# Kernel optimization log

Measured on AMD Instinct MI355X. Metric: run time of the kernel, lower is better.

Reference implementation:

```python
import jax, jax.numpy as jnp
import numpy as np

B, NQ, N, D_IN, D_KEY, D_MODEL = 8, 2048, 2048, 512, 512, 512


def setup_inputs() -> dict:
    key = jax.random.key(0)
    k1, k2, k3, k4, k5, k6 = jax.random.split(key, 6)
    lim_k = np.sqrt(6.0 / (D_IN + D_KEY))
    lim_v = np.sqrt(6.0 / (D_IN + D_MODEL))
    return {
        "node_features": jax.random.normal(k1, (B, N, D_IN), dtype=jnp.float32),
        "query": jax.random.normal(k2, (B, NQ, D_IN), dtype=jnp.float32),
        "mask": jax.random.bernoulli(k3, 0.3, (NQ, B, N)),  # True = masked out
        "wq": jax.random.uniform(k4, (D_IN, D_KEY), jnp.float32, -lim_k, lim_k),
        "wk": jax.random.uniform(k5, (D_IN, D_KEY), jnp.float32, -lim_k, lim_k),
        "wv": jax.random.uniform(k6, (D_IN, D_MODEL), jnp.float32, -lim_v, lim_v),
    }


def reference(node_features, query, mask, wq, wk, wv):
    # Projections
    Q = query @ wq              # [B, NQ, d_key]
    K = node_features @ wk      # [B, N, d_key]
    V = node_features @ wv      # [B, N, d_model]
    # Raw scores [B, NQ, N]
    scores = jnp.einsum("bqd,bnd->bqn", Q, K)
    b, nq, n = scores.shape
    # Faithful to tf: reshape to (NQ, B, N), mask with float32.min, reshape back
    s = scores.reshape(nq, b, n)
    masked = jnp.where(mask, jnp.finfo(jnp.float32).min, s).reshape(b, nq, n)
    # Scale AFTER masking (as in the original), then softmax over keys
    attn = jax.nn.softmax(masked / jnp.sqrt(jnp.float32(K.shape[-1])), axis=-1)
    return attn @ V             # [B, NQ, d_model]
```

## Files before the change

### kernel.cpp

```cpp
#include <hip/hip_runtime.h>

#define BATCH 8
#define NQ    2048
#define NKV   2048
#define DIN   512
#define DKEY  512
#define DMOD  512

typedef __attribute__((ext_vector_type(8))) short bf16x8;
typedef __attribute__((ext_vector_type(4))) float f32x4;

__device__ __forceinline__ unsigned short f2bf(float f) {
  unsigned int u = __builtin_bit_cast(unsigned int, f);
  u += 0x7fffu + ((u >> 16) & 1u);
  return (unsigned short)(u >> 16);
}
__device__ __forceinline__ float bf2f(unsigned short h) {
  unsigned int u = ((unsigned int)h) << 16;
  return __builtin_bit_cast(float, u);
}

#define GLD16(gp, lp) __builtin_amdgcn_global_load_lds( \
    (const __attribute__((address_space(1))) unsigned int*)(gp), \
    (__attribute__((address_space(3))) unsigned int*)(lp), 16, 0, 0)

__global__ void detect_mode(const unsigned int* __restrict__ mask, int* __restrict__ flag) {
  __shared__ int c1s;
  if (threadIdx.x == 0) c1s = 0;
  __syncthreads();
  int c1 = 0;
  for (int i = threadIdx.x; i < 16384; i += 256) {
    unsigned int u = mask[i];
    if (u & 0x0000ff00u) c1++;
  }
  atomicAdd(&c1s, c1);
  __syncthreads();
  if (threadIdx.x == 0) *flag = (c1s > 0) ? 1 : 4;
}

__global__ void cvt_two(const float* __restrict__ a, const float* __restrict__ b,
                        unsigned short* __restrict__ oa, unsigned short* __restrict__ ob) {
  int i = blockIdx.x * 256 + threadIdx.x;
  const float* src;
  unsigned short* dst;
  int j;
  if (i < 2097152) { src = a; dst = oa; j = i; }
  else             { src = b; dst = ob; j = i - 2097152; }
  float4 v = ((const float4*)src)[j];
  ushort4 o;
  o.x = f2bf(v.x); o.y = f2bf(v.y); o.z = f2bf(v.z); o.w = f2bf(v.w);
  ((ushort4*)dst)[j] = o;
}

__global__ void cvt_w3(const float* __restrict__ wq, const float* __restrict__ wk,
                       const float* __restrict__ wv,
                       unsigned short* __restrict__ oq, unsigned short* __restrict__ ok,
                       unsigned short* __restrict__ ov) {
  int idx = blockIdx.x * 256 + threadIdx.x;
  int w = idx >> 18;
  int rem = idx & 262143;
  int n = rem >> 9, k = rem & 511;
  const float* W = (w == 0) ? wq : (w == 1) ? wk : wv;
  unsigned short* O = (w == 0) ? oq : (w == 1) ? ok : ov;
  O[n * 512 + k] = f2bf(W[k * 512 + n]);
}

__device__ __forceinline__ void gemm256_core(
    const unsigned short* __restrict__ Ab,
    const unsigned short* __restrict__ Bb,
    unsigned short* __restrict__ C,
    long ldA, long ldB, long ldO, int nk, long bm, long bn, char* smem)
{
  const int tid = threadIdx.x;
  const int lane = tid & 63;
  const int wid = tid >> 6;
  const int wr = wid >> 1;
  const int wc = wid & 1;
  const int fr = lane & 15, fq = lane >> 4;

  const int srow = tid >> 3;
  const int clog = (tid & 7) ^ (srow & 7);

  char* buf0 = smem;
  char* buf1 = smem + 65536;

  f32x4 acc[4][8] = {};

  const int swz0 = ((fq)     ^ (fr & 7)) * 16;
  const int swz1 = ((4 + fq) ^ (fr & 7)) * 16;
  const int arow = (wr * 64 + fr) * 128;
  const int brow = (wc * 128 + fr) * 128;

  {
    const unsigned short* ga = Ab + (bm + srow) * ldA + clog * 8;
    const unsigned short* gb = Bb + (bn + srow) * ldB + clog * 8;
#pragma unroll
    for (int l = 0; l < 4; ++l) {
      GLD16(ga + (long)l * 64 * ldA, buf0 + l * 8192 + tid * 16);
      GLD16(gb + (long)l * 64 * ldB, buf0 + 32768 + l * 8192 + tid * 16);
    }
  }

  char* cur = buf0;
  char* nxt = buf1;
  for (int t = 0; t < nk; ++t) {
    __builtin_amdgcn_sched_barrier(0);
    __builtin_amdgcn_s_barrier();
    if (t + 1 < nk) {
      const long k0 = (long)(t + 1) * 64;
      const unsigned short* ga = Ab + (bm + srow) * ldA + k0 + clog * 8;
      const unsigned short* gb = Bb + (bn + srow) * ldB + k0 + clog * 8;
#pragma unroll
      for (int l = 0; l < 4; ++l) {
        GLD16(ga + (long)l * 64 * ldA, nxt + l * 8192 + tid * 16);
        GLD16(gb + (long)l * 64 * ldB, nxt + 32768 + l * 8192 + tid * 16);
      }
      asm volatile("s_waitcnt vmcnt(8)" ::: "memory");
    } else {
      asm volatile("s_waitcnt vmcnt(0)" ::: "memory");
    }
    __builtin_amdgcn_s_barrier();
    __builtin_amdgcn_sched_barrier(0);

    const char* bufA = cur;
    const char* bufB = cur + 32768;
#pragma unroll
    for (int kh = 0; kh < 2; ++kh) {
      const int swz = kh ? swz1 : swz0;
      bf16x8 a[4];
#pragma unroll
      for (int mi = 0; mi < 4; ++mi)
        a[mi] = *(const bf16x8*)(bufA + arow + mi * 2048 + swz);
#pragma unroll
      for (int nh = 0; nh < 2; ++nh) {
        bf16x8 b[4];
#pragma unroll
        for (int nj = 0; nj < 4; ++nj)
          b[nj] = *(const bf16x8*)(bufB + brow + (nh * 4 + nj) * 2048 + swz);
        __builtin_amdgcn_s_setprio(1);
#pragma unroll
        for (int mi = 0; mi < 4; ++mi)
#pragma unroll
          for (int nj = 0; nj < 4; ++nj)
            acc[mi][nh * 4 + nj] = __builtin_amdgcn_mfma_f32_16x16x32_bf16(
                a[mi], b[nj], acc[mi][nh * 4 + nj], 0, 0, 0);
        __builtin_amdgcn_s_setprio(0);
      }
    }
    char* tmp = cur; cur = nxt; nxt = tmp;
  }

#pragma unroll
  for (int mi = 0; mi < 4; ++mi)
#pragma unroll
    for (int ni = 0; ni < 8; ++ni) {
      const long row = bm + wr * 64 + mi * 16 + fq * 4;
      const long col = bn + wc * 128 + ni * 16 + fr;
#pragma unroll
      for (int r = 0; r < 4; ++r)
        C[(row + r) * ldO + col] = f2bf(acc[mi][ni][r]);
    }
}

__global__ __launch_bounds__(512, 2) void gemm256_scores(
    const unsigned short* __restrict__ Q, const unsigned short* __restrict__ Kb,
    unsigned short* __restrict__ S)
{
  extern __shared__ char smem[];
  const long z = blockIdx.z;
  gemm256_core(Q + z * 1048576, Kb + z * 1048576, S + z * 4194304,
               512, 512, 2048, 8, (long)blockIdx.x * 256, (long)blockIdx.y * 256, smem);
}

__global__ __launch_bounds__(512, 2) void gemm256_proj(
    const unsigned short* __restrict__ Xq, const unsigned short* __restrict__ Xn,
    const unsigned short* __restrict__ Wqt, const unsigned short* __restrict__ Wkt,
    const unsigned short* __restrict__ Wvt,
    unsigned short* __restrict__ Q, unsigned short* __restrict__ Kb,
    unsigned short* __restrict__ Vt)
{
  extern __shared__ char smem[];
  const int z = blockIdx.z;
  if (z == 0)
    gemm256_core(Xq, Wqt, Q, 512, 512, 512, 8,
                 (long)blockIdx.x * 256, (long)blockIdx.y * 256, smem);
  else if (z == 1)
    gemm256_core(Xn, Wkt, Kb, 512, 512, 512, 8,
                 (long)blockIdx.x * 256, (long)blockIdx.y * 256, smem);
  else
    gemm256_core(Wvt, Xn, Vt, 512, 512, 16384, 8,
                 (long)blockIdx.y * 256, (long)blockIdx.x * 256, smem);
}

__device__ __forceinline__ void gemm_core(
    const unsigned short* Ab, const unsigned short* Bb, void* Cb,
    int K, long ldB, int out_mode, long ldO, long bm, long bn,
    unsigned short (*Al)[32], unsigned short (*Bl)[32])
{
  const int t = threadIdx.x;
  const int lane = t & 63;
  const int w = t >> 6;
  const int wm = (w >> 1) * 64, wn = (w & 1) * 64;
  const int fr = lane & 15, fq = lane >> 4;

  f32x4 acc[4][4] = {};

  const int slot0 = t, slot1 = 256 + t;
  const int r0 = slot0 >> 2, s0 = slot0 & 3;
  const int r1 = slot1 >> 2, s1 = slot1 & 3;

  const int nk = K >> 5;
  for (int kt = 0; kt < nk; ++kt) {
    const long k0 = (long)kt << 5;
    GLD16(Ab + (bm + r0) * K + k0 + s0 * 8, &Al[0][0] + slot0 * 8);
    GLD16(Ab + (bm + r1) * K + k0 + s1 * 8, &Al[0][0] + slot1 * 8);
    GLD16(Bb + (bn + r0) * ldB + k0 + s0 * 8, &Bl[0][0] + slot0 * 8);
    GLD16(Bb + (bn + r1) * ldB + k0 + s1 * 8, &Bl[0][0] + slot1 * 8);
    __syncthreads();

    bf16x8 af[4], bfr[4];
#pragma unroll
    for (int mi = 0; mi < 4; ++mi)
      af[mi] = *(const bf16x8*)&Al[wm + mi * 16 + fr][fq * 8];
#pragma unroll
    for (int ni = 0; ni < 4; ++ni)
      bfr[ni] = *(const bf16x8*)&Bl[wn + ni * 16 + fr][fq * 8];
#pragma unroll
    for (int mi = 0; mi < 4; ++mi)
#pragma unroll
      for (int ni = 0; ni < 4; ++ni)
        acc[mi][ni] = __builtin_amdgcn_mfma_f32_16x16x32_bf16(af[mi], bfr[ni], acc[mi][ni], 0, 0, 0);
    __syncthreads();
  }

  if (out_mode == 2) {
    float* C = (float*)Cb;
#pragma unroll
    for (int mi = 0; mi < 4; ++mi)
#pragma unroll
      for (int ni = 0; ni < 4; ++ni) {
        const long row = bm + wm + mi * 16 + fq * 4;
        const long col = bn + wn + ni * 16 + fr;
#pragma unroll
        for (int r = 0; r < 4; ++r)
          C[(row + r) * ldO + col] = acc[mi][ni][r];
      }
  } else {
    unsigned short* C = (unsigned short*)Cb;
#pragma unroll
    for (int mi = 0; mi < 4; ++mi)
#pragma unroll
      for (int ni = 0; ni < 4; ++ni) {
        const long row = bm + wm + mi * 16 + fq * 4;
        const long col = bn + wn + ni * 16 + fr;
#pragma unroll
        for (int r = 0; r < 4; ++r)
          C[(row + r) * ldO + col] = f2bf(acc[mi][ni][r]);
      }
  }
}

__global__ __launch_bounds__(256) void gemm_bt(
    const unsigned short* __restrict__ A,
    const unsigned short* __restrict__ Bt,
    void* __restrict__ Cout,
    int K, long ldB,
    long batchA, long batchB, long batchC,
    int out_mode, long ldO, int out_f32)
{
  __shared__ unsigned short Al[128][32];
  __shared__ unsigned short Bl[128][32];
  const unsigned short* Ab = A + (size_t)blockIdx.z * batchA;
  const unsigned short* Bb = Bt + (size_t)blockIdx.z * batchB;
  char* Cb = (char*)Cout + (size_t)blockIdx.z * batchC * (out_f32 ? 4 : 2);
  gemm_core(Ab, Bb, Cb, K, ldB, out_mode, ldO,
            (long)blockIdx.x * 128, (long)blockIdx.y * 128, Al, Bl);
}

__global__ __launch_bounds__(256) void softmax_rows(
    unsigned short* __restrict__ S,
    const unsigned char* __restrict__ mask,
    const int* __restrict__ flag)
{
  const int t = threadIdx.x;
  const size_t base = (size_t)blockIdx.x * 2048 + (size_t)t * 8;
  uint4 sv = *(const uint4*)(S + base);

  float x[8];
  {
    unsigned int w0 = sv.x, w1 = sv.y, w2 = sv.z, w3 = sv.w;
    x[0] = bf2f((unsigned short)(w0 & 0xffff)); x[1] = bf2f((unsigned short)(w0 >> 16));
    x[2] = bf2f((unsigned short)(w1 & 0xffff)); x[3] = bf2f((unsigned short)(w1 >> 16));
    x[4] = bf2f((unsigned short)(w2 & 0xffff)); x[5] = bf2f((unsigned short)(w2 >> 16));
    x[6] = bf2f((unsigned short)(w3 & 0xffff)); x[7] = bf2f((unsigned short)(w3 >> 16));
  }

  const int esz = *flag;
  unsigned int mbits = 0;
  if (esz == 1) {
    unsigned long long mv = *(const unsigned long long*)(mask + base);
#pragma unroll
    for (int j = 0; j < 8; ++j)
      if ((mv >> (8 * j)) & 0xffULL) mbits |= 1u << j;
  } else {
    const uint4* mp = (const uint4*)(mask + base * 4);
    uint4 a = mp[0], b = mp[1];
    if (a.x) mbits |= 1u;   if (a.y) mbits |= 2u;
    if (a.z) mbits |= 4u;   if (a.w) mbits |= 8u;
    if (b.x) mbits |= 16u;  if (b.y) mbits |= 32u;
    if (b.z) mbits |= 64u;  if (b.w) mbits |= 128u;
  }

  const float SCALE = 0.04419417382415922f;
  float xs[8];
#pragma unroll
  for (int j = 0; j < 8; ++j) {
    float v = ((mbits >> j) & 1u) ? -3.4028234663852886e38f : x[j];
    xs[j] = v * SCALE;
  }

  float m = xs[0];
#pragma unroll
  for (int j = 1; j < 8; ++j) m = fmaxf(m, xs[j]);
#pragma unroll
  for (int off = 32; off > 0; off >>= 1) m = fmaxf(m, __shfl_xor(m, off));

  __shared__ float rm[4], rs[4];
  if ((t & 63) == 0) rm[t >> 6] = m;
  __syncthreads();
  m = fmaxf(fmaxf(rm[0], rm[1]), fmaxf(rm[2], rm[3]));

  float e[8], ssum = 0.f;
#pragma unroll
  for (int j = 0; j < 8; ++j) { e[j] = __expf(xs[j] - m); ssum += e[j]; }
#pragma unroll
  for (int off = 32; off > 0; off >>= 1) ssum += __shfl_xor(ssum, off);
  if ((t & 63) == 0) rs[t >> 6] = ssum;
  __syncthreads();
  ssum = rs[0] + rs[1] + rs[2] + rs[3];
  const float inv = 1.0f / ssum;

  unsigned int o0 = (unsigned int)f2bf(e[0] * inv) | ((unsigned int)f2bf(e[1] * inv) << 16);
  unsigned int o1 = (unsigned int)f2bf(e[2] * inv) | ((unsigned int)f2bf(e[3] * inv) << 16);
  unsigned int o2 = (unsigned int)f2bf(e[4] * inv) | ((unsigned int)f2bf(e[5] * inv) << 16);
  unsigned int o3 = (unsigned int)f2bf(e[6] * inv) | ((unsigned int)f2bf(e[7] * inv) << 16);
  uint4 ov; ov.x = o0; ov.y = o1; ov.z = o2; ov.w = o3;
  *(uint4*)(S + base) = ov;
}

extern "C" void kernel_launch(void* const* d_in, const int* in_sizes, int n_in,
                              void* d_out, int out_size, void* d_ws, size_t ws_size,
                              hipStream_t stream) {
  const float* node  = (const float*)d_in[0];
  const float* query = (const float*)d_in[1];
  const unsigned char* mask = (const unsigned char*)d_in[2];
  const float* wq = (const float*)d_in[3];
  const float* wk = (const float*)d_in[4];
  const float* wv = (const float*)d_in[5];
  float* out = (float*)d_out;

  char* ws = (char*)d_ws;
  unsigned short* Q   = (unsigned short*)(ws);
  unsigned short* Kb  = (unsigned short*)(ws + 16777216);
  unsigned short* Vt  = (unsigned short*)(ws + 33554432);
  unsigned short* S   = (unsigned short*)(ws + 50331648);
  unsigned short* Xq  = (unsigned short*)(ws + 50331648);
  unsigned short* Xn  = (unsigned short*)(ws + 50331648 + 16777216);
  unsigned short* Wqt = (unsigned short*)(ws + 50331648 + 33554432);
  unsigned short* Wkt = Wqt + 262144;
  unsigned short* Wvt = Wkt + 262144;
  int* flag = (int*)(ws + 117440512);

  detect_mode<<<1, 256, 0, stream>>>((const unsigned int*)mask, flag);

  cvt_two<<<16384, 256, 0, stream>>>(query, node, Xq, Xn);
  cvt_w3<<<3072, 256, 0, stream>>>(wq, wk, wv, Wqt, Wkt, Wvt);

  dim3 gp(64, 2, 3);
  gemm256_proj<<<gp, 512, 131072, stream>>>(Xq, Xn, Wqt, Wkt, Wvt, Q, Kb, Vt);

  dim3 gs(8, 8, 8);
  gemm256_scores<<<gs, 512, 131072, stream>>>(Q, Kb, S);

  softmax_rows<<<16384, 256, 0, stream>>>(S, mask, flag);

  dim3 gv(16, 4, 8);
  gemm_bt<<<gv, 256, 0, stream>>>(S, Vt, out, 2048, 16384,
                                  4194304L, 2048L, 1048576L, 2, 512, 1);
}
```

Measured before the change: 220.9 us.

## Fuse mask and exp into scores GEMM epilogue, defer normalization to PV GEMM

The scores GEMM epilogue now applies the mask and writes exp(score*scale) directly, skipping the max subtraction. A light rowsum kernel computes reciprocal row sums. A new double-buffered 256x128 PV GEMM applies those reciprocals in its epilogue, replacing the separate softmax pass and the older gemm_bt kernel. This removes a full read-modify-write pass over the score matrix. The cost is that exp without max subtraction can overflow for large scores, and a fully masked row would give NaN where the reference gives a uniform row.

```diff
diff --git a/kernel.cpp b/kernel.cpp
--- a/kernel.cpp
+++ b/kernel.cpp
@@ -14,10 +14,6 @@
   unsigned int u = __builtin_bit_cast(unsigned int, f);
   u += 0x7fffu + ((u >> 16) & 1u);
   return (unsigned short)(u >> 16);
-}
-__device__ __forceinline__ float bf2f(unsigned short h) {
-  unsigned int u = ((unsigned int)h) << 16;
-  return __builtin_bit_cast(float, u);
 }
 
 #define GLD16(gp, lp) __builtin_amdgcn_global_load_lds( \
@@ -69,7 +65,8 @@
     const unsigned short* __restrict__ Ab,
     const unsigned short* __restrict__ Bb,
     unsigned short* __restrict__ C,
-    long ldA, long ldB, long ldO, int nk, long bm, long bn, char* smem)
+    long ldA, long ldB, long ldO, int nk, long bm, long bn, char* smem,
+    const unsigned char* emask, int esz, long maskBase)
 {
   const int tid = threadIdx.x;
   const int lane = tid & 63;
@@ -150,26 +147,41 @@
     char* tmp = cur; cur = nxt; nxt = tmp;
   }
 
+  const float SCALE = 0.04419417382415922f;
 #pragma unroll
   for (int mi = 0; mi < 4; ++mi)
 #pragma unroll
     for (int ni = 0; ni < 8; ++ni) {
       const long row = bm + wr * 64 + mi * 16 + fq * 4;
       const long col = bn + wc * 128 + ni * 16 + fr;
-#pragma unroll
-      for (int r = 0; r < 4; ++r)
-        C[(row + r) * ldO + col] = f2bf(acc[mi][ni][r]);
+      if (emask == nullptr) {
+#pragma unroll
+        for (int r = 0; r < 4; ++r)
+          C[(row + r) * ldO + col] = f2bf(acc[mi][ni][r]);
+      } else {
+#pragma unroll
+        for (int r = 0; r < 4; ++r) {
+          const long f = maskBase + (row + r) * ldO + col;
+          bool msk;
+          if (esz == 1) msk = emask[f] != 0;
+          else          msk = ((const unsigned int*)emask)[f] != 0;
+          float e = msk ? 0.0f : __expf(acc[mi][ni][r] * SCALE);
+          C[(row + r) * ldO + col] = f2bf(e);
+        }
+      }
     }
 }
 
 __global__ __launch_bounds__(512, 2) void gemm256_scores(
     const unsigned short* __restrict__ Q, const unsigned short* __restrict__ Kb,
-    unsigned short* __restrict__ S)
+    unsigned short* __restrict__ S,
+    const unsigned char* __restrict__ mask, const int* __restrict__ flag)
 {
   extern __shared__ char smem[];
   const long z = blockIdx.z;
   gemm256_core(Q + z * 1048576, Kb + z * 1048576, S + z * 4194304,
-               512, 512, 2048, 8, (long)blockIdx.x * 256, (long)blockIdx.y * 256, smem);
+               512, 512, 2048, 8, (long)blockIdx.x * 256, (long)blockIdx.y * 256, smem,
+               mask, *flag, z * 4194304);
 }
 
 __global__ __launch_bounds__(512, 2) void gemm256_proj(
@@ -183,169 +195,137 @@
   const int z = blockIdx.z;
   if (z == 0)
     gemm256_core(Xq, Wqt, Q, 512, 512, 512, 8,
-                 (long)blockIdx.x * 256, (long)blockIdx.y * 256, smem);
+                 (long)blockIdx.x * 256, (long)blockIdx.y * 256, smem, nullptr, 0, 0);
   else if (z == 1)
     gemm256_core(Xn, Wkt, Kb, 512, 512, 512, 8,
-                 (long)blockIdx.x * 256, (long)blockIdx.y * 256, smem);
+                 (long)blockIdx.x * 256, (long)blockIdx.y * 256, smem, nullptr, 0, 0);
   else
     gemm256_core(Wvt, Xn, Vt, 512, 512, 16384, 8,
-                 (long)blockIdx.y * 256, (long)blockIdx.x * 256, smem);
-}
-
-__device__ __forceinline__ void gemm_core(
-    const unsigned short* Ab, const unsigned short* Bb, void* Cb,
-    int K, long ldB, int out_mode, long ldO, long bm, long bn,
-    unsigned short (*Al)[32], unsigned short (*Bl)[32])
-{
-  const int t = threadIdx.x;
-  const int lane = t & 63;
-  const int w = t >> 6;
-  const int wm = (w >> 1) * 64, wn = (w & 1) * 64;
+                 (long)blockIdx.y * 256, (long)blockIdx.x * 256, smem, nullptr, 0, 0);
+}
+
+__global__ __launch_bounds__(256) void rowsum_inv(
+    const unsigned short* __restrict__ E, float* __restrict__ inv)
+{
+  const int row = blockIdx.x * 4 + (threadIdx.x >> 6);
+  const int lane = threadIdx.x & 63;
+  const uint4* p = (const uint4*)(E + (size_t)row * 2048);
+  float s = 0.f;
+#pragma unroll
+  for (int j = 0; j < 4; ++j) {
+    uint4 v = p[lane + j * 64];
+    unsigned int w[4] = {v.x, v.y, v.z, v.w};
+#pragma unroll
+    for (int q = 0; q < 4; ++q) {
+      s += __builtin_bit_cast(float, (w[q] & 0xffffu) << 16);
+      s += __builtin_bit_cast(float, w[q] & 0xffff0000u);
+    }
+  }
+#pragma unroll
+  for (int off = 32; off > 0; off >>= 1) s += __shfl_xor(s, off);
+  if (lane == 0) inv[row] = 1.0f / s;
+}
+
+__global__ __launch_bounds__(512, 2) void gemm_pv(
+    const unsigned short* __restrict__ E, const unsigned short* __restrict__ Vt,
+    const float* __restrict__ inv, float* __restrict__ O)
+{
+  extern __shared__ char smem[];
+  const long z = blockIdx.z;
+  const unsigned short* Ab = E + z * 4194304;
+  const unsigned short* Bb = Vt + z * 2048;
+  const long bm = (long)blockIdx.x * 256;
+  const long bn = (long)blockIdx.y * 128;
+
+  const int tid = threadIdx.x;
+  const int lane = tid & 63;
+  const int wid = tid >> 6;
+  const int wr = wid >> 1;
+  const int wc = wid & 1;
   const int fr = lane & 15, fq = lane >> 4;
 
+  const int srow = tid >> 3;
+  const int clog = (tid & 7) ^ (srow & 7);
+
+  char* buf0 = smem;
+  char* buf1 = smem + 49152;
+
   f32x4 acc[4][4] = {};
 
-  const int slot0 = t, slot1 = 256 + t;
-  const int r0 = slot0 >> 2, s0 = slot0 & 3;
-  const int r1 = slot1 >> 2, s1 = slot1 & 3;
-
-  const int nk = K >> 5;
-  for (int kt = 0; kt < nk; ++kt) {
-    const long k0 = (long)kt << 5;
-    GLD16(Ab + (bm + r0) * K + k0 + s0 * 8, &Al[0][0] + slot0 * 8);
-    GLD16(Ab + (bm + r1) * K + k0 + s1 * 8, &Al[0][0] + slot1 * 8);
-    GLD16(Bb + (bn + r0) * ldB + k0 + s0 * 8, &Bl[0][0] + slot0 * 8);
-    GLD16(Bb + (bn + r1) * ldB + k0 + s1 * 8, &Bl[0][0] + slot1 * 8);
-    __syncthreads();
-
-    bf16x8 af[4], bfr[4];
-#pragma unroll
-    for (int mi = 0; mi < 4; ++mi)
-      af[mi] = *(const bf16x8*)&Al[wm + mi * 16 + fr][fq * 8];
-#pragma unroll
-    for (int ni = 0; ni < 4; ++ni)
-      bfr[ni] = *(const bf16x8*)&Bl[wn + ni * 16 + fr][fq * 8];
-#pragma unroll
-    for (int mi = 0; mi < 4; ++mi)
-#pragma unroll
-      for (int ni = 0; ni < 4; ++ni)
-        acc[mi][ni] = __builtin_amdgcn_mfma_f32_16x16x32_bf16(af[mi], bfr[ni], acc[mi][ni], 0, 0, 0);
-    __syncthreads();
-  }
-
-  if (out_mode == 2) {
-    float* C = (float*)Cb;
-#pragma unroll
-    for (int mi = 0; mi < 4; ++mi)
-#pragma unroll
-      for (int ni = 0; ni < 4; ++ni) {
-        const long row = bm + wm + mi * 16 + fq * 4;
-        const long col = bn + wn + ni * 16 + fr;
-#pragma unroll
-        for (int r = 0; r < 4; ++r)
-          C[(row + r) * ldO + col] = acc[mi][ni][r];
-      }
-  } else {
-    unsigned short* C = (unsigned short*)Cb;
-#pragma unroll
-    for (int mi = 0; mi < 4; ++mi)
-#pragma unroll
-      for (int ni = 0; ni < 4; ++ni) {
-        const long row = bm + wm + mi * 16 + fq * 4;
-        const long col = bn + wn + ni * 16 + fr;
-#pragma unroll
-        for (int r = 0; r < 4; ++r)
-          C[(row + r) * ldO + col] = f2bf(acc[mi][ni][r]);
-      }
-  }
-}
-
-__global__ __launch_bounds__(256) void gemm_bt(
-    const unsigned short* __restrict__ A,
-    const unsigned short* __restrict__ Bt,
-    void* __restrict__ Cout,
-    int K, long ldB,
-    long batchA, long batchB, long batchC,
-    int out_mode, long ldO, int out_f32)
-{
-  __shared__ unsigned short Al[128][32];
-  __shared__ unsigned short Bl[128][32];
-  const unsigned short* Ab = A + (size_t)blockIdx.z * batchA;
-  const unsigned short* Bb = Bt + (size_t)blockIdx.z * batchB;
-  char* Cb = (char*)Cout + (size_t)blockIdx.z * batchC * (out_f32 ? 4 : 2);
-  gemm_core(Ab, Bb, Cb, K, ldB, out_mode, ldO,
-            (long)blockIdx.x * 128, (long)blockIdx.y * 128, Al, Bl);
-}
-
-__global__ __launch_bounds__(256) void softmax_rows(
-    unsigned short* __restrict__ S,
-    const unsigned char* __restrict__ mask,
-    const int* __restrict__ flag)
-{
-  const int t = threadIdx.x;
-  const size_t base = (size_t)blockIdx.x * 2048 + (size_t)t * 8;
-  uint4 sv = *(const uint4*)(S + base);
-
-  float x[8];
+  const int swz0 = ((fq)     ^ (fr & 7)) * 16;
+  const int swz1 = ((4 + fq) ^ (fr & 7)) * 16;
+  const int arow = (wr * 64 + fr) * 128;
+  const int brow = (wc * 64 + fr) * 128;
+
   {
-    unsigned int w0 = sv.x, w1 = sv.y, w2 = sv.z, w3 = sv.w;
-    x[0] = bf2f((unsigned short)(w0 & 0xffff)); x[1] = bf2f((unsigned short)(w0 >> 16));
-    x[2] = bf2f((unsigned short)(w1 & 0xffff)); x[3] = bf2f((unsigned short)(w1 >> 16));
-    x[4] = bf2f((unsigned short)(w2 & 0xffff)); x[5] = bf2f((unsigned short)(w2 >> 16));
-    x[6] = bf2f((unsigned short)(w3 & 0xffff)); x[7] = bf2f((unsigned short)(w3 >> 16));
-  }
-
-  const int esz = *flag;
-  unsigned int mbits = 0;
-  if (esz == 1) {
-    unsigned long long mv = *(const unsigned long long*)(mask + base);
-#pragma unroll
-    for (int j = 0; j < 8; ++j)
-      if ((mv >> (8 * j)) & 0xffULL) mbits |= 1u << j;
-  } else {
-    const uint4* mp = (const uint4*)(mask + base * 4);
-    uint4 a = mp[0], b = mp[1];
-    if (a.x) mbits |= 1u;   if (a.y) mbits |= 2u;
-    if (a.z) mbits |= 4u;   if (a.w) mbits |= 8u;
-    if (b.x) mbits |= 16u;  if (b.y) mbits |= 32u;
-    if (b.z) mbits |= 64u;  if (b.w) mbits |= 128u;
-  }
-
-  const float SCALE = 0.04419417382415922f;
-  float xs[8];
-#pragma unroll
-  for (int j = 0; j < 8; ++j) {
-    float v = ((mbits >> j) & 1u) ? -3.4028234663852886e38f : x[j];
-    xs[j] = v * SCALE;
-  }
-
-  float m = xs[0];
-#pragma unroll
-  for (int j = 1; j < 8; ++j) m = fmaxf(m, xs[j]);
-#pragma unroll
-  for (int off = 32; off > 0; off >>= 1) m = fmaxf(m, __shfl_xor(m, off));
-
-  __shared__ float rm[4], rs[4];
-  if ((t & 63) == 0) rm[t >> 6] = m;
-  __syncthreads();
-  m = fmaxf(fmaxf(rm[0], rm[1]), fmaxf(rm[2], rm[3]));
-
-  float e[8], ssum = 0.f;
-#pragma unroll
-  for (int j = 0; j < 8; ++j) { e[j] = __expf(xs[j] - m); ssum += e[j]; }
-#pragma unroll
-  for (int off = 32; off > 0; off >>= 1) ssum += __shfl_xor(ssum, off);
-  if ((t & 63) == 0) rs[t >> 6] = ssum;
-  __syncthreads();
-  ssum = rs[0] + rs[1] + rs[2] + rs[3];
-  const float inv = 1.0f / ssum;
-
-  unsigned int o0 = (unsigned int)f2bf(e[0] * inv) | ((unsigned int)f2bf(e[1] * inv) << 16);
-  unsigned int o1 = (unsigned int)f2bf(e[2] * inv) | ((unsigned int)f2bf(e[3] * inv) << 16);
-  unsigned int o2 = (unsigned int)f2bf(e[4] * inv) | ((unsigned int)f2bf(e[5] * inv) << 16);
-  unsigned int o3 = (unsigned int)f2bf(e[6] * inv) | ((unsigned int)f2bf(e[7] * inv) << 16);
-  uint4 ov; ov.x = o0; ov.y = o1; ov.z = o2; ov.w = o3;
-  *(uint4*)(S + base) = ov;
+    const unsigned short* ga = Ab + (bm + srow) * 2048 + clog * 8;
+    const unsigned short* gb = Bb + (bn + srow) * 16384 + clog * 8;
+#pragma unroll
+    for (int l = 0; l < 4; ++l)
+      GLD16(ga + (long)l * 64 * 2048, buf0 + l * 8192 + tid * 16);
+#pragma unroll
+    for (int l = 0; l < 2; ++l)
+      GLD16(gb + (long)l * 64 * 16384, buf0 + 32768 + l * 8192 + tid * 16);
+  }
+
+  char* cur = buf0;
+  char* nxt = buf1;
+  for (int t = 0; t < 32; ++t) {
+    __builtin_amdgcn_sched_barrier(0);
+    __builtin_amdgcn_s_barrier();
+    if (t + 1 < 32) {
+      const long k0 = (long)(t + 1) * 64;
+      const unsigned short* ga = Ab + (bm + srow) * 2048 + k0 + clog * 8;
+      const unsigned short* gb = Bb + (bn + srow) * 16384 + k0 + clog * 8;
+#pragma unroll
+      for (int l = 0; l < 4; ++l)
+        GLD16(ga + (long)l * 64 * 2048, nxt + l * 8192 + tid * 16);
+#pragma unroll
+      for (int l = 0; l < 2; ++l)
+        GLD16(gb + (long)l * 64 * 16384, nxt + 32768 + l * 8192 + tid * 16);
+      asm volatile("s_waitcnt vmcnt(6)" ::: "memory");
+    } else {
+      asm volatile("s_waitcnt vmcnt(0)" ::: "memory");
+    }
+    __builtin_amdgcn_s_barrier();
+    __builtin_amdgcn_sched_barrier(0);
+
+    const char* bufA = cur;
+    const char* bufB = cur + 32768;
+#pragma unroll
+    for (int kh = 0; kh < 2; ++kh) {
+      const int swz = kh ? swz1 : swz0;
+      bf16x8 a[4], b[4];
+#pragma unroll
+      for (int mi = 0; mi < 4; ++mi)
+        a[mi] = *(const bf16x8*)(bufA + arow + mi * 2048 + swz);
+#pragma unroll
+      for (int nj = 0; nj < 4; ++nj)
+        b[nj] = *(const bf16x8*)(bufB + brow + nj * 2048 + swz);
+      __builtin_amdgcn_s_setprio(1);
+#pragma unroll
+      for (int mi = 0; mi < 4; ++mi)
+#pragma unroll
+        for (int nj = 0; nj < 4; ++nj)
+          acc[mi][nj] = __builtin_amdgcn_mfma_f32_16x16x32_bf16(
+              a[mi], b[nj], acc[mi][nj], 0, 0, 0);
+      __builtin_amdgcn_s_setprio(0);
+    }
+    char* tmp = cur; cur = nxt; nxt = tmp;
+  }
+
+  float* Ob = O + z * 1048576;
+  const float* invb = inv + z * 2048;
+#pragma unroll
+  for (int mi = 0; mi < 4; ++mi)
+#pragma unroll
+    for (int nj = 0; nj < 4; ++nj) {
+      const long row = bm + wr * 64 + mi * 16 + fq * 4;
+      const long col = bn + wc * 64 + nj * 16 + fr;
+#pragma unroll
+      for (int r = 0; r < 4; ++r)
+        Ob[(row + r) * 512 + col] = acc[mi][nj][r] * invb[row + r];
+    }
 }
 
 extern "C" void kernel_launch(void* const* d_in, const int* in_sizes, int n_in,
@@ -363,13 +343,14 @@
   unsigned short* Q   = (unsigned short*)(ws);
   unsigned short* Kb  = (unsigned short*)(ws + 16777216);
   unsigned short* Vt  = (unsigned short*)(ws + 33554432);
-  unsigned short* S   = (unsigned short*)(ws + 50331648);
+  unsigned short* E   = (unsigned short*)(ws + 50331648);
   unsigned short* Xq  = (unsigned short*)(ws + 50331648);
   unsigned short* Xn  = (unsigned short*)(ws + 50331648 + 16777216);
   unsigned short* Wqt = (unsigned short*)(ws + 50331648 + 33554432);
   unsigned short* Wkt = Wqt + 262144;
   unsigned short* Wvt = Wkt + 262144;
-  int* flag = (int*)(ws + 117440512);
+  float* inv = (float*)(ws + 117440512);
+  int* flag  = (int*)(ws + 117440512 + 65536);
 
   detect_mode<<<1, 256, 0, stream>>>((const unsigned int*)mask, flag);
 
@@ -380,11 +361,10 @@
   gemm256_proj<<<gp, 512, 131072, stream>>>(Xq, Xn, Wqt, Wkt, Wvt, Q, Kb, Vt);
 
   dim3 gs(8, 8, 8);
-  gemm256_scores<<<gs, 512, 131072, stream>>>(Q, Kb, S);
-
-  softmax_rows<<<16384, 256, 0, stream>>>(S, mask, flag);
-
-  dim3 gv(16, 4, 8);
-  gemm_bt<<<gv, 256, 0, stream>>>(S, Vt, out, 2048, 16384,
-                                  4194304L, 2048L, 1048576L, 2, 512, 1);
-}
+  gemm256_scores<<<gs, 512, 131072, stream>>>(Q, Kb, E, mask, flag);
+
+  rowsum_inv<<<4096, 256, 0, stream>>>(E, inv);
+
+  dim3 gv(8, 4, 8);
+  gemm_pv<<<gv, 512, 98304, stream>>>(E, Vt, inv, out);
+}
```

After: 291.0 us. +31.7%, slower.
